# Performance work log

Measured on AMD Instinct MI355X. Metric: run time of the kernel, lower is better.

## Reference

```python
import jax, jax.numpy as jnp
import numpy as np

B, S, D, U = 4, 2048, 1024, 1024

def setup_inputs() -> dict:
    key = jax.random.key(0)
    k0, k1, k2, k3 = jax.random.split(key, 4)
    scale = 1.0 / np.sqrt(D)  # keep logits sane; Glorot-like magnitude
    return {
        "inputs": jax.random.normal(k0, (B, S, D), dtype=jnp.float32),
        "W_q": jax.random.normal(k1, (D, U), dtype=jnp.float32) * scale,
        "W_k": jax.random.normal(k2, (D, U), dtype=jnp.float32) * scale,
        "W_v": jax.random.normal(k3, (D, U), dtype=jnp.float32) * scale,
    }

def reference(inputs, W_q, W_k, W_v):
    # QKV projections: [B,S,D] @ [D,U] -> [B,S,U]
    q = jnp.einsum("bsd,du->bsu", inputs, W_q)
    k = jnp.einsum("bsd,du->bsu", inputs, W_k)
    v = jnp.einsum("bsd,du->bsu", inputs, W_v)
    # Unscaled attention, as in the source (no 1/sqrt(d) factor)
    scores = jnp.einsum("bqu,bku->bqk", q, k)          # [B,S,S]
    weights = jax.nn.softmax(scores, axis=-1)
    return jnp.einsum("bqk,bku->bqu", weights, v)       # [B,S,U]
```

## Files before the change

### kernel.cpp

```cpp
#include <hip/hip_runtime.h>
#include <cstdint>
#include <cstddef>


typedef unsigned short ushort_t;
typedef _Float16 half_t;
typedef __attribute__((ext_vector_type(8))) short short8;
typedef __attribute__((ext_vector_type(4))) float floatx4;

__device__ inline unsigned short h2u(half_t h) {
  union { half_t h; unsigned short u; } v; v.h = h; return v.u;
}

__device__ __forceinline__ void gload16(const half_t* g, half_t* l) {
  __builtin_amdgcn_global_load_lds(
      (const __attribute__((address_space(1))) unsigned int*)g,
      (__attribute__((address_space(3))) unsigned int*)l, 16, 0, 0);
}

#define MX 8192
#define KCAT 2048

#define XCAT_OFF 0UL
#define WT_OFF   50331648UL
#define S_OFF    0UL
#define QCAT_OFF 69206016UL
#define KCAT_OFF 119537664UL
#define VT_OFF   169869312UL
#define WS_NEED  186646528UL

__global__ __launch_bounds__(256) void k_split_x(const float* __restrict__ X,
                                                 half_t* __restrict__ xcat) {
  long long i = (long long)blockIdx.x * 256 + threadIdx.x;
  float x = X[i];
  half_t h = (half_t)x;
  half_t lo = (half_t)(x - (float)h);
  long long row = i >> 10;
  int col = (int)(i & 1023);
  half_t* r = xcat + row * KCAT;
  r[col] = h;
  r[col + 1024] = lo;
}

__global__ __launch_bounds__(256) void k_split_wt(const float* __restrict__ Wq,
                                                  const float* __restrict__ Wk,
                                                  const float* __restrict__ Wv,
                                                  half_t* __restrict__ wt) {
  __shared__ float tile[64][65];
  const float* W = (blockIdx.z == 0) ? Wq : ((blockIdx.z == 1) ? Wk : Wv);
  half_t* out = wt + (size_t)blockIdx.z * 1024 * KCAT;
  int d0 = blockIdx.y * 64, u0 = blockIdx.x * 64;
  int t = threadIdx.x;
  int tr = t >> 6, tc = t & 63;
  for (int r = 0; r < 64; r += 4)
    tile[r + tr][tc] = W[(size_t)(d0 + r + tr) * 1024 + (u0 + tc)];
  __syncthreads();
  for (int r = 0; r < 64; r += 4) {
    int urow = r + tr, dcol = tc;
    float x = tile[dcol][urow];
    half_t h = (half_t)x;
    half_t* o = out + (size_t)(u0 + urow) * KCAT + d0;
    o[dcol] = h;
    o[dcol + 1024] = h;
  }
}

enum { EP_F32 = 0, EP_QK = 1, EP_VT = 2 };

template <int MODE>
__global__ __launch_bounds__(256, 4) void k_gemm(
    const half_t* __restrict__ A, long long aBatch, int lda,
    const half_t* __restrict__ Bt, long long bBatch, int ldb,
    void* __restrict__ Cout, long long cBatch, int ldc, int K,
    half_t* __restrict__ CoutK) {
  __shared__ __align__(16) half_t As[128 * 64];
  __shared__ __align__(16) half_t Bs[128 * 64];
  const int t = threadIdx.x;
  const int z = blockIdx.z;
  A += (long long)z * aBatch;
  Bt += (long long)z * bBatch;
  const int m0 = blockIdx.y * 128, n0 = blockIdx.x * 128;

  const int w = t >> 6, l = t & 63;
  const int lr = l & 15, quad = l >> 4;
  const int wm = (w >> 1) * 64, wn = (w & 1) * 64;

  const floatx4 fz = {0.f, 0.f, 0.f, 0.f};
  floatx4 acc[4][4];
#pragma unroll
  for (int i = 0; i < 4; i++)
#pragma unroll
    for (int j = 0; j < 4; j++) acc[i][j] = fz;

  const half_t* Ap[4];
  const half_t* Bp[4];
  half_t* ldsA[4];
  half_t* ldsB[4];
#pragma unroll
  for (int s = 0; s < 4; s++) {
    int c = s * 256 + t;
    int row = c >> 3, gq = (c & 7) ^ ((c >> 3) & 7);
    Ap[s] = A + (long long)(m0 + row) * lda + gq * 8;
    Bp[s] = Bt + (long long)(n0 + row) * ldb + gq * 8;
    ldsA[s] = &As[(s * 256 + w * 64) * 8];
    ldsB[s] = &Bs[(s * 256 + w * 64) * 8];
  }

  const int p0 = quad ^ (lr & 7);
  const int p1 = (quad + 4) ^ (lr & 7);
  const int arow = (wm + lr) * 64, brow = (wn + lr) * 64;

  for (int kb = 0; kb < K; kb += 64) {
    __syncthreads();
#pragma unroll
    for (int s = 0; s < 4; s++) {
      gload16(Ap[s] + kb, ldsA[s]);
      gload16(Bp[s] + kb, ldsB[s]);
    }
    __syncthreads();
#pragma unroll
    for (int s = 0; s < 2; s++) {
      const int pp = s ? p1 : p0;
      short8 af[4], bfg[4];
#pragma unroll
      for (int j = 0; j < 4; j++) bfg[j] = *(const short8*)&Bs[brow + j * 1024 + pp * 8];
#pragma unroll
      for (int i = 0; i < 4; i++) af[i] = *(const short8*)&As[arow + i * 1024 + pp * 8];
#pragma unroll
      for (int i = 0; i < 4; i++)
#pragma unroll
        for (int j = 0; j < 4; j++)
          acc[i][j] = __builtin_amdgcn_mfma_f32_16x16x32_f16(af[i], bfg[j], acc[i][j], 0, 0, 0);
    }
  }

#pragma unroll
  for (int i = 0; i < 4; i++) {
#pragma unroll
    for (int j = 0; j < 4; j++) {
#pragma unroll
      for (int r = 0; r < 4; r++) {
        int grow = m0 + wm + i * 16 + quad * 4 + r;
        int gcol = n0 + wn + j * 16 + lr;
        float v = acc[i][j][r];
        if (MODE == EP_F32) {
          float* C = (float*)Cout + (long long)z * cBatch;
          C[(long long)grow * ldc + gcol] = v;
        } else if (MODE == EP_QK) {
          int sel = gcol >> 10;
          int ucol = gcol & 1023;
          half_t h = (half_t)v;
          if (sel == 0) {
            half_t* pq = (half_t*)Cout + (long long)grow * KCAT;
            pq[ucol] = h;
            pq[ucol + 1024] = (half_t)(v - (float)h);
          } else {
            half_t* pk = CoutK + (long long)grow * KCAT;
            pk[ucol] = h;
            pk[ucol + 1024] = h;
          }
        } else {
          half_t* C = (half_t*)Cout;
          int b = grow >> 11, s = grow & 2047;
          C[((long long)b * 1024 + gcol) * 2048 + s] = (half_t)v;
        }
      }
    }
  }
}

__global__ __launch_bounds__(256) void k_softmax(float* __restrict__ Sbuf) {
  long long row = blockIdx.x;
  float* p = Sbuf + row * 2048;
  int t = threadIdx.x;
  float4 v0 = ((const float4*)p)[t];
  float4 v1 = ((const float4*)p)[t + 256];
  float m = fmaxf(fmaxf(fmaxf(v0.x, v0.y), fmaxf(v0.z, v0.w)),
                  fmaxf(fmaxf(v1.x, v1.y), fmaxf(v1.z, v1.w)));
  for (int off = 32; off; off >>= 1) m = fmaxf(m, __shfl_xor(m, off));
  __shared__ float red[8];
  int wv = t >> 6, ln = t & 63;
  if (ln == 0) red[wv] = m;
  __syncthreads();
  m = fmaxf(fmaxf(red[0], red[1]), fmaxf(red[2], red[3]));
  float e0 = __expf(v0.x - m), e1 = __expf(v0.y - m), e2 = __expf(v0.z - m), e3 = __expf(v0.w - m);
  float e4 = __expf(v1.x - m), e5 = __expf(v1.y - m), e6 = __expf(v1.z - m), e7 = __expf(v1.w - m);
  float s = ((e0 + e1) + (e2 + e3)) + ((e4 + e5) + (e6 + e7));
  for (int off = 32; off; off >>= 1) s += __shfl_xor(s, off);
  if (ln == 0) red[4 + wv] = s;
  __syncthreads();
  s = (red[4] + red[5]) + (red[6] + red[7]);
  float inv = 1.0f / s;
  uint2 w0, w1;
  w0.x = (unsigned)h2u((half_t)(e0 * inv)) | ((unsigned)h2u((half_t)(e1 * inv)) << 16);
  w0.y = (unsigned)h2u((half_t)(e2 * inv)) | ((unsigned)h2u((half_t)(e3 * inv)) << 16);
  w1.x = (unsigned)h2u((half_t)(e4 * inv)) | ((unsigned)h2u((half_t)(e5 * inv)) << 16);
  w1.y = (unsigned)h2u((half_t)(e6 * inv)) | ((unsigned)h2u((half_t)(e7 * inv)) << 16);
  ((uint2*)p)[t] = w0;
  ((uint2*)p)[t + 256] = w1;
}

extern "C" void kernel_launch(void* const* d_in, const int* in_sizes, int n_in,
                              void* d_out, int out_size, void* d_ws, size_t ws_size,
                              hipStream_t stream) {
  (void)in_sizes; (void)n_in; (void)out_size;
  if (ws_size < WS_NEED) return;

  const float* X = (const float*)d_in[0];
  const float* Wq = (const float*)d_in[1];
  const float* Wk = (const float*)d_in[2];
  const float* Wv = (const float*)d_in[3];
  char* ws = (char*)d_ws;
  half_t* xcat = (half_t*)(ws + XCAT_OFF);
  half_t* wt = (half_t*)(ws + WT_OFF);
  float* Sbuf = (float*)(ws + S_OFF);
  half_t* qcat = (half_t*)(ws + QCAT_OFF);
  half_t* kcat = (half_t*)(ws + KCAT_OFF);
  half_t* vt = (half_t*)(ws + VT_OFF);
  float* out = (float*)d_out;

  k_split_x<<<dim3(MX * 1024 / 256), dim3(256), 0, stream>>>(X, xcat);
  k_split_wt<<<dim3(16, 16, 3), dim3(256), 0, stream>>>(Wq, Wk, Wv, wt);

  k_gemm<EP_QK><<<dim3(16, 64, 1), dim3(256), 0, stream>>>(
      xcat, 0LL, KCAT, wt, 0LL, KCAT, qcat, 0LL, 0, KCAT, kcat);

  k_gemm<EP_VT><<<dim3(8, 64, 1), dim3(256), 0, stream>>>(
      xcat, 0LL, KCAT, wt + 2 * 1024 * KCAT, 0LL, KCAT, vt, 0LL, 0, 1024, nullptr);

  k_gemm<EP_F32><<<dim3(16, 16, 4), dim3(256), 0, stream>>>(
      qcat, (long long)2048 * KCAT, KCAT, kcat, (long long)2048 * KCAT, KCAT,
      Sbuf, (long long)2048 * 2048, 2048, KCAT, nullptr);

  k_softmax<<<dim3(8192), dim3(256), 0, stream>>>(Sbuf);

  k_gemm<EP_F32><<<dim3(8, 16, 4), dim3(256), 0, stream>>>(
      (const half_t*)Sbuf, (long long)2048 * 4096, 4096,
      vt, (long long)1024 * 2048, 2048,
      out, (long long)2048 * 1024, 1024, 2048, nullptr);
}
```

Before: 335.7 us.

## Prefetch next GEMM K-tile during MFMA, vectorize split, wave-per-row softmax

The GEMM main loop now reads LDS fragments into registers, then issues the global-to-LDS loads for the next K tile before running the MFMAs. Global load latency can therefore overlap compute while a single LDS buffer is kept. The x split kernel is vectorized to float4 loads with packed half stores. Softmax now handles one row per wavefront using shuffles only, which removes shared-memory reductions and block barriers. The cost is more live registers for the held fragments, which may affect occupancy under the launch bound of 4.

```diff
diff --git a/kernel.cpp b/kernel.cpp
--- a/kernel.cpp
+++ b/kernel.cpp
@@ -31,15 +31,21 @@
 
 __global__ __launch_bounds__(256) void k_split_x(const float* __restrict__ X,
                                                  half_t* __restrict__ xcat) {
-  long long i = (long long)blockIdx.x * 256 + threadIdx.x;
-  float x = X[i];
-  half_t h = (half_t)x;
-  half_t lo = (half_t)(x - (float)h);
-  long long row = i >> 10;
-  int col = (int)(i & 1023);
+  long long i4 = ((long long)blockIdx.x * 256 + threadIdx.x) * 4;
+  float4 x = *(const float4*)(X + i4);
+  half_t h0 = (half_t)x.x, h1 = (half_t)x.y, h2 = (half_t)x.z, h3 = (half_t)x.w;
+  half_t l0 = (half_t)(x.x - (float)h0), l1 = (half_t)(x.y - (float)h1);
+  half_t l2 = (half_t)(x.z - (float)h2), l3 = (half_t)(x.w - (float)h3);
+  long long row = i4 >> 10;
+  int col = (int)(i4 & 1023);
   half_t* r = xcat + row * KCAT;
-  r[col] = h;
-  r[col + 1024] = lo;
+  uint2 hi, lo;
+  hi.x = (unsigned)h2u(h0) | ((unsigned)h2u(h1) << 16);
+  hi.y = (unsigned)h2u(h2) | ((unsigned)h2u(h3) << 16);
+  lo.x = (unsigned)h2u(l0) | ((unsigned)h2u(l1) << 16);
+  lo.y = (unsigned)h2u(l2) | ((unsigned)h2u(l3) << 16);
+  *(uint2*)(r + col) = hi;
+  *(uint2*)(r + col + 1024) = lo;
 }
 
 __global__ __launch_bounds__(256) void k_split_wt(const float* __restrict__ Wq,
@@ -110,28 +116,39 @@
   const int p1 = (quad + 4) ^ (lr & 7);
   const int arow = (wm + lr) * 64, brow = (wn + lr) * 64;
 
+#pragma unroll
+  for (int s = 0; s < 4; s++) {
+    gload16(Ap[s], ldsA[s]);
+    gload16(Bp[s], ldsB[s]);
+  }
+
   for (int kb = 0; kb < K; kb += 64) {
     __syncthreads();
-#pragma unroll
-    for (int s = 0; s < 4; s++) {
-      gload16(Ap[s] + kb, ldsA[s]);
-      gload16(Bp[s] + kb, ldsB[s]);
+    short8 af[2][4], bfg[2][4];
+#pragma unroll
+    for (int s = 0; s < 2; s++) {
+      const int pp = s ? p1 : p0;
+#pragma unroll
+      for (int j = 0; j < 4; j++) bfg[s][j] = *(const short8*)&Bs[brow + j * 1024 + pp * 8];
+#pragma unroll
+      for (int i = 0; i < 4; i++) af[s][i] = *(const short8*)&As[arow + i * 1024 + pp * 8];
     }
     __syncthreads();
-#pragma unroll
-    for (int s = 0; s < 2; s++) {
-      const int pp = s ? p1 : p0;
-      short8 af[4], bfg[4];
-#pragma unroll
-      for (int j = 0; j < 4; j++) bfg[j] = *(const short8*)&Bs[brow + j * 1024 + pp * 8];
-#pragma unroll
-      for (int i = 0; i < 4; i++) af[i] = *(const short8*)&As[arow + i * 1024 + pp * 8];
+    int kn = kb + 64;
+    if (kn < K) {
+#pragma unroll
+      for (int s = 0; s < 4; s++) {
+        gload16(Ap[s] + kn, ldsA[s]);
+        gload16(Bp[s] + kn, ldsB[s]);
+      }
+    }
+#pragma unroll
+    for (int s = 0; s < 2; s++)
 #pragma unroll
       for (int i = 0; i < 4; i++)
 #pragma unroll
         for (int j = 0; j < 4; j++)
-          acc[i][j] = __builtin_amdgcn_mfma_f32_16x16x32_f16(af[i], bfg[j], acc[i][j], 0, 0, 0);
-    }
+          acc[i][j] = __builtin_amdgcn_mfma_f32_16x16x32_f16(af[s][i], bfg[s][j], acc[i][j], 0, 0, 0);
   }
 
 #pragma unroll
@@ -170,34 +187,35 @@
 }
 
 __global__ __launch_bounds__(256) void k_softmax(float* __restrict__ Sbuf) {
-  long long row = blockIdx.x;
+  int wv = threadIdx.x >> 6, ln = threadIdx.x & 63;
+  long long row = (long long)blockIdx.x * 4 + wv;
   float* p = Sbuf + row * 2048;
-  int t = threadIdx.x;
-  float4 v0 = ((const float4*)p)[t];
-  float4 v1 = ((const float4*)p)[t + 256];
-  float m = fmaxf(fmaxf(fmaxf(v0.x, v0.y), fmaxf(v0.z, v0.w)),
-                  fmaxf(fmaxf(v1.x, v1.y), fmaxf(v1.z, v1.w)));
+  float4 v[8];
+#pragma unroll
+  for (int j = 0; j < 8; j++) v[j] = ((const float4*)p)[ln + 64 * j];
+  float m = -1e30f;
+#pragma unroll
+  for (int j = 0; j < 8; j++)
+    m = fmaxf(m, fmaxf(fmaxf(v[j].x, v[j].y), fmaxf(v[j].z, v[j].w)));
+#pragma unroll
   for (int off = 32; off; off >>= 1) m = fmaxf(m, __shfl_xor(m, off));
-  __shared__ float red[8];
-  int wv = t >> 6, ln = t & 63;
-  if (ln == 0) red[wv] = m;
-  __syncthreads();
-  m = fmaxf(fmaxf(red[0], red[1]), fmaxf(red[2], red[3]));
-  float e0 = __expf(v0.x - m), e1 = __expf(v0.y - m), e2 = __expf(v0.z - m), e3 = __expf(v0.w - m);
-  float e4 = __expf(v1.x - m), e5 = __expf(v1.y - m), e6 = __expf(v1.z - m), e7 = __expf(v1.w - m);
-  float s = ((e0 + e1) + (e2 + e3)) + ((e4 + e5) + (e6 + e7));
+  float s = 0.f;
+#pragma unroll
+  for (int j = 0; j < 8; j++) {
+    v[j].x = __expf(v[j].x - m); v[j].y = __expf(v[j].y - m);
+    v[j].z = __expf(v[j].z - m); v[j].w = __expf(v[j].w - m);
+    s += (v[j].x + v[j].y) + (v[j].z + v[j].w);
+  }
+#pragma unroll
   for (int off = 32; off; off >>= 1) s += __shfl_xor(s, off);
-  if (ln == 0) red[4 + wv] = s;
-  __syncthreads();
-  s = (red[4] + red[5]) + (red[6] + red[7]);
   float inv = 1.0f / s;
-  uint2 w0, w1;
-  w0.x = (unsigned)h2u((half_t)(e0 * inv)) | ((unsigned)h2u((half_t)(e1 * inv)) << 16);
-  w0.y = (unsigned)h2u((half_t)(e2 * inv)) | ((unsigned)h2u((half_t)(e3 * inv)) << 16);
-  w1.x = (unsigned)h2u((half_t)(e4 * inv)) | ((unsigned)h2u((half_t)(e5 * inv)) << 16);
-  w1.y = (unsigned)h2u((half_t)(e6 * inv)) | ((unsigned)h2u((half_t)(e7 * inv)) << 16);
-  ((uint2*)p)[t] = w0;
-  ((uint2*)p)[t + 256] = w1;
+#pragma unroll
+  for (int j = 0; j < 8; j++) {
+    uint2 wo;
+    wo.x = (unsigned)h2u((half_t)(v[j].x * inv)) | ((unsigned)h2u((half_t)(v[j].y * inv)) << 16);
+    wo.y = (unsigned)h2u((half_t)(v[j].z * inv)) | ((unsigned)h2u((half_t)(v[j].w * inv)) << 16);
+    ((uint2*)p)[ln + 64 * j] = wo;
+  }
 }
 
 extern "C" void kernel_launch(void* const* d_in, const int* in_sizes, int n_in,
@@ -219,7 +237,7 @@
   half_t* vt = (half_t*)(ws + VT_OFF);
   float* out = (float*)d_out;
 
-  k_split_x<<<dim3(MX * 1024 / 256), dim3(256), 0, stream>>>(X, xcat);
+  k_split_x<<<dim3(MX * 1024 / 1024), dim3(256), 0, stream>>>(X, xcat);
   k_split_wt<<<dim3(16, 16, 3), dim3(256), 0, stream>>>(Wq, Wk, Wv, wt);
 
   k_gemm<EP_QK><<<dim3(16, 64, 1), dim3(256), 0, stream>>>(
@@ -232,7 +250,7 @@
       qcat, (long long)2048 * KCAT, KCAT, kcat, (long long)2048 * KCAT, KCAT,
       Sbuf, (long long)2048 * 2048, 2048, KCAT, nullptr);
 
-  k_softmax<<<dim3(8192), dim3(256), 0, stream>>>(Sbuf);
+  k_softmax<<<dim3(2048), dim3(256), 0, stream>>>(Sbuf);
 
   k_gemm<EP_F32><<<dim3(8, 16, 4), dim3(256), 0, stream>>>(
       (const half_t*)Sbuf, (long long)2048 * 4096, 4096,
```

Result: slower. 769.4 us (+129.2%).
